# Optimization experiments

Measured on AMD Instinct MI355X. Metric: run time of the kernel, lower is better.

The kernel has to match this reference:

```python
import jax, jax.numpy as jnp
import numpy as np


def setup_inputs() -> dict:
    key = jax.random.key(0)
    k1, k2 = jax.random.split(key)
    qs = jax.random.normal(k1, (64, 32, 128), dtype=jnp.float32)   # (n_queries, n_query_tokens, dim)
    ps = jax.random.normal(k2, (64, 1024, 128), dtype=jnp.float32)  # (n_docs, n_doc_tokens, dim)
    return {"qs": qs, "ps": ps}


def reference(qs, ps):
    # ColBERT MaxSim: for each (query b, doc c), sum over query tokens of the
    # max similarity against all doc tokens.
    # scores[b,c,n,s] = sum_d qs[b,n,d] * ps[c,s,d]
    sim = jnp.einsum('bnd,csd->bcns', qs, ps)  # (n_q, n_d, tok_q, tok_d)
    scores = sim.max(axis=3).sum(axis=2)       # (n_q, n_d)
    return scores
```

## Files before the change

kernel.cpp:

```cpp
#include <hip/hip_runtime.h>
#include <stdint.h>


typedef __bf16 bf16x8 __attribute__((ext_vector_type(8)));
typedef float floatx16 __attribute__((ext_vector_type(16)));

#define QS_N (64u * 32u * 128u)
#define PS_N (64u * 1024u * 128u)

__device__ ushort g_bf[QS_N + PS_N];

__global__ __launch_bounds__(256) void cvt_kernel(const float* __restrict__ qs,
                                                  const float* __restrict__ ps) {
  const int nq4 = QS_N / 4;
  const int n4 = (QS_N + PS_N) / 4;
  int i = blockIdx.x * 256 + threadIdx.x;
  if (i >= n4) return;
  float4 f = (i < nq4) ? ((const float4*)qs)[i] : ((const float4*)ps)[i - nq4];
  union { ushort4 s; struct { __bf16 a, b, c, d; } h; } o;
  o.h.a = (__bf16)f.x; o.h.b = (__bf16)f.y; o.h.c = (__bf16)f.z; o.h.d = (__bf16)f.w;
  ((ushort4*)g_bf)[i] = o.s;
}

__device__ inline float rmax16(const floatx16& a) {
  float m0 = fmaxf(fmaxf(a[0], a[1]), fmaxf(a[2], a[3]));
  float m1 = fmaxf(fmaxf(a[4], a[5]), fmaxf(a[6], a[7]));
  float m2 = fmaxf(fmaxf(a[8], a[9]), fmaxf(a[10], a[11]));
  float m3 = fmaxf(fmaxf(a[12], a[13]), fmaxf(a[14], a[15]));
  return fmaxf(fmaxf(m0, m1), fmaxf(m2, m3));
}

typedef __attribute__((address_space(1))) const void gas_t;
typedef __attribute__((address_space(3))) void las_t;
__device__ inline void gload_lds16(const ushort* g, ushort* l) {
  __builtin_amdgcn_global_load_lds((gas_t*)g, (las_t*)l, 16, 0, 0);
}

#define ZERO16 {0, 0, 0, 0, 0, 0, 0, 0, 0, 0, 0, 0, 0, 0, 0, 0}

__global__ __launch_bounds__(256) void maxsim_kernel(float* __restrict__ out) {
  const ushort* qsb = g_bf;
  const ushort* psb = g_bf + QS_N;

  const int lane = threadIdx.x & 63;
  const int wave = threadIdx.x >> 6;

  const int xcd = blockIdx.x & 7;
  const int slot = blockIdx.x >> 3;
  const int c = xcd * 8 + (slot >> 3);
  const int bg = slot & 7;
  const int qb0 = bg * 8 + wave * 2;

  const int row = lane & 31;
  const int hi8 = (lane >> 5) * 8;

  bf16x8 qf[2][8];
#pragma unroll
  for (int bb = 0; bb < 2; ++bb) {
    const ushort* q = qsb + ((qb0 + bb) * 32 + row) * 128 + hi8;
#pragma unroll
    for (int k = 0; k < 8; ++k)
      qf[bb][k] = *(const bf16x8*)(q + k * 16);
  }

  __shared__ __align__(16) ushort lds_p[2][4096];

  const int pg_lane = (c * 1024 + row) * 128 + hi8;

#pragma unroll
  for (int jj = 0; jj < 2; ++jj) {
    const int j = wave * 2 + jj;
    gload_lds16(psb + pg_lane + j * 16, &lds_p[0][j * 512]);
  }
  __syncthreads();

  float vmax0 = -3.4e38f, vmax1 = -3.4e38f;
  int cb = 0;

#pragma unroll 1
  for (int t = 0; t < 32; ++t) {
    if (t < 31) {
      const int soff = (t + 1) * 32 * 128;
#pragma unroll
      for (int jj = 0; jj < 2; ++jj) {
        const int j = wave * 2 + jj;
        gload_lds16(psb + pg_lane + soff + j * 16, &lds_p[cb ^ 1][j * 512]);
      }
    }
    const ushort* lp = &lds_p[cb][0] + lane * 8;
    floatx16 acc0 = ZERO16, acc1 = ZERO16;
#pragma unroll
    for (int k = 0; k < 8; ++k) {
      bf16x8 af = *(const bf16x8*)(lp + k * 512);
      acc0 = __builtin_amdgcn_mfma_f32_32x32x16_bf16(af, qf[0][k], acc0, 0, 0, 0);
      acc1 = __builtin_amdgcn_mfma_f32_32x32x16_bf16(af, qf[1][k], acc1, 0, 0, 0);
    }
    vmax0 = fmaxf(vmax0, rmax16(acc0));
    vmax1 = fmaxf(vmax1, rmax16(acc1));
    __syncthreads();
    cb ^= 1;
  }

  vmax0 = fmaxf(vmax0, __shfl_xor(vmax0, 32, 64));
  vmax1 = fmaxf(vmax1, __shfl_xor(vmax1, 32, 64));
#pragma unroll
  for (int o = 16; o > 0; o >>= 1) {
    vmax0 += __shfl_xor(vmax0, o, 64);
    vmax1 += __shfl_xor(vmax1, o, 64);
  }
  if (lane == 0) {
    out[(qb0 + 0) * 64 + c] = vmax0;
    out[(qb0 + 1) * 64 + c] = vmax1;
  }
}

extern "C" void kernel_launch(void* const* d_in, const int* in_sizes, int n_in,
                              void* d_out, int out_size, void* d_ws, size_t ws_size,
                              hipStream_t stream) {
  const float* qs = (const float*)d_in[0];
  const float* ps = (const float*)d_in[1];
  float* out = (float*)d_out;
  (void)d_ws; (void)ws_size;

  const int n4 = (int)((QS_N + PS_N) / 4);
  cvt_kernel<<<(n4 + 255) / 256, 256, 0, stream>>>(qs, ps);
  maxsim_kernel<<<dim3(512), dim3(256), 0, stream>>>(out);
}
```

Baseline: 111.5 us.

## Fuse fp32-to-bf16 conversion into the MaxSim kernel and drop the separate pass

Removes the standalone conversion kernel and its bf16 scratch buffer. The MaxSim kernel now loads fp32 queries and documents directly and converts them to bf16 in registers. Document tiles are prefetched into registers during the MFMA loop and written to LDS after compute, replacing async global-to-LDS loads. This trades an extra launch and a full round trip of the converted data for doubled redundant fp32 traffic across blocks that share a document, and for register-staged prefetching.

```diff
diff --git a/kernel.cpp b/kernel.cpp
--- a/kernel.cpp
+++ b/kernel.cpp
@@ -5,21 +5,11 @@
 typedef __bf16 bf16x8 __attribute__((ext_vector_type(8)));
 typedef float floatx16 __attribute__((ext_vector_type(16)));
 
-#define QS_N (64u * 32u * 128u)
-#define PS_N (64u * 1024u * 128u)
-
-__device__ ushort g_bf[QS_N + PS_N];
-
-__global__ __launch_bounds__(256) void cvt_kernel(const float* __restrict__ qs,
-                                                  const float* __restrict__ ps) {
-  const int nq4 = QS_N / 4;
-  const int n4 = (QS_N + PS_N) / 4;
-  int i = blockIdx.x * 256 + threadIdx.x;
-  if (i >= n4) return;
-  float4 f = (i < nq4) ? ((const float4*)qs)[i] : ((const float4*)ps)[i - nq4];
-  union { ushort4 s; struct { __bf16 a, b, c, d; } h; } o;
-  o.h.a = (__bf16)f.x; o.h.b = (__bf16)f.y; o.h.c = (__bf16)f.z; o.h.d = (__bf16)f.w;
-  ((ushort4*)g_bf)[i] = o.s;
+__device__ inline bf16x8 cvt8(const float4& a, const float4& b) {
+  bf16x8 r;
+  r[0] = (__bf16)a.x; r[1] = (__bf16)a.y; r[2] = (__bf16)a.z; r[3] = (__bf16)a.w;
+  r[4] = (__bf16)b.x; r[5] = (__bf16)b.y; r[6] = (__bf16)b.z; r[7] = (__bf16)b.w;
+  return r;
 }
 
 __device__ inline float rmax16(const floatx16& a) {
@@ -30,18 +20,11 @@
   return fmaxf(fmaxf(m0, m1), fmaxf(m2, m3));
 }
 
-typedef __attribute__((address_space(1))) const void gas_t;
-typedef __attribute__((address_space(3))) void las_t;
-__device__ inline void gload_lds16(const ushort* g, ushort* l) {
-  __builtin_amdgcn_global_load_lds((gas_t*)g, (las_t*)l, 16, 0, 0);
-}
-
 #define ZERO16 {0, 0, 0, 0, 0, 0, 0, 0, 0, 0, 0, 0, 0, 0, 0, 0}
 
-__global__ __launch_bounds__(256) void maxsim_kernel(float* __restrict__ out) {
-  const ushort* qsb = g_bf;
-  const ushort* psb = g_bf + QS_N;
-
+__global__ __launch_bounds__(256) void maxsim_kernel(const float* __restrict__ qs,
+                                                     const float* __restrict__ ps,
+                                                     float* __restrict__ out) {
   const int lane = threadIdx.x & 63;
   const int wave = threadIdx.x >> 6;
 
@@ -57,20 +40,26 @@
   bf16x8 qf[2][8];
 #pragma unroll
   for (int bb = 0; bb < 2; ++bb) {
-    const ushort* q = qsb + ((qb0 + bb) * 32 + row) * 128 + hi8;
+    const float* q = qs + ((qb0 + bb) * 32 + row) * 128 + hi8;
 #pragma unroll
-    for (int k = 0; k < 8; ++k)
-      qf[bb][k] = *(const bf16x8*)(q + k * 16);
+    for (int k = 0; k < 8; ++k) {
+      float4 a = *(const float4*)(q + k * 16);
+      float4 b = *(const float4*)(q + k * 16 + 4);
+      qf[bb][k] = cvt8(a, b);
+    }
   }
 
   __shared__ __align__(16) ushort lds_p[2][4096];
 
-  const int pg_lane = (c * 1024 + row) * 128 + hi8;
+  const float* pg = ps + (c * 1024 + row) * 128 + hi8;
 
 #pragma unroll
   for (int jj = 0; jj < 2; ++jj) {
     const int j = wave * 2 + jj;
-    gload_lds16(psb + pg_lane + j * 16, &lds_p[0][j * 512]);
+    const float* src = pg + j * 16;
+    float4 a = *(const float4*)src;
+    float4 b = *(const float4*)(src + 4);
+    *(bf16x8*)(&lds_p[0][j * 512 + lane * 8]) = cvt8(a, b);
   }
   __syncthreads();
 
@@ -79,13 +68,13 @@
 
 #pragma unroll 1
   for (int t = 0; t < 32; ++t) {
+    float4 Fa0, Fb0, Fa1, Fb1;
     if (t < 31) {
-      const int soff = (t + 1) * 32 * 128;
-#pragma unroll
-      for (int jj = 0; jj < 2; ++jj) {
-        const int j = wave * 2 + jj;
-        gload_lds16(psb + pg_lane + soff + j * 16, &lds_p[cb ^ 1][j * 512]);
-      }
+      const float* src = pg + (t + 1) * 32 * 128 + (wave * 2) * 16;
+      Fa0 = *(const float4*)src;
+      Fb0 = *(const float4*)(src + 4);
+      Fa1 = *(const float4*)(src + 16);
+      Fb1 = *(const float4*)(src + 20);
     }
     const ushort* lp = &lds_p[cb][0] + lane * 8;
     floatx16 acc0 = ZERO16, acc1 = ZERO16;
@@ -97,6 +86,11 @@
     }
     vmax0 = fmaxf(vmax0, rmax16(acc0));
     vmax1 = fmaxf(vmax1, rmax16(acc1));
+    if (t < 31) {
+      ushort* dst = &lds_p[cb ^ 1][(wave * 2) * 512 + lane * 8];
+      *(bf16x8*)dst = cvt8(Fa0, Fb0);
+      *(bf16x8*)(dst + 512) = cvt8(Fa1, Fb1);
+    }
     __syncthreads();
     cb ^= 1;
   }
@@ -122,7 +116,5 @@
   float* out = (float*)d_out;
   (void)d_ws; (void)ws_size;
 
-  const int n4 = (int)((QS_N + PS_N) / 4);
-  cvt_kernel<<<(n4 + 255) / 256, 256, 0, stream>>>(qs, ps);
-  maxsim_kernel<<<dim3(512), dim3(256), 0, stream>>>(out);
+  maxsim_kernel<<<dim3(512), dim3(256), 0, stream>>>(qs, ps, out);
 }
```

After: 124.5 us. 11.7% more time.

## Split doc tokens across wave pairs, each wave holds four query blocks

Applied to the files above, without the earlier changes.

Each wave now keeps four query blocks in registers instead of two. Pairs of waves take different 32-token halves of a 64-token doc tile, so each LDS A-fragment load feeds four MFMAs and the loop runs 16 iterations instead of 32. A shared-memory cross-wave max reduction merges the two halves before the final sum. Per-wave register pressure doubles, which is pinned with empty asm constraints, and the LDS buffer doubles in size, which may reduce occupancy.

```diff
diff --git a/kernel.cpp b/kernel.cpp
--- a/kernel.cpp
+++ b/kernel.cpp
@@ -9,6 +9,8 @@
 #define PS_N (64u * 1024u * 128u)
 
 __device__ ushort g_bf[QS_N + PS_N];
+
+union FU { bf16x8 v; uint4 u; };
 
 __global__ __launch_bounds__(256) void cvt_kernel(const float* __restrict__ qs,
                                                   const float* __restrict__ ps) {
@@ -49,68 +51,93 @@
   const int slot = blockIdx.x >> 3;
   const int c = xcd * 8 + (slot >> 3);
   const int bg = slot & 7;
-  const int qb0 = bg * 8 + wave * 2;
+
+  const int qgrp = wave >> 1;
+  const int usel = wave & 1;
+  const int qb0 = bg * 8 + qgrp * 4;
 
   const int row = lane & 31;
   const int hi8 = (lane >> 5) * 8;
 
-  bf16x8 qf[2][8];
+  uint4 qf[4][8];
 #pragma unroll
-  for (int bb = 0; bb < 2; ++bb) {
+  for (int bb = 0; bb < 4; ++bb) {
     const ushort* q = qsb + ((qb0 + bb) * 32 + row) * 128 + hi8;
 #pragma unroll
     for (int k = 0; k < 8; ++k)
-      qf[bb][k] = *(const bf16x8*)(q + k * 16);
+      qf[bb][k] = *(const uint4*)(q + k * 16);
   }
+#pragma unroll
+  for (int bb = 0; bb < 4; ++bb)
+#pragma unroll
+    for (int k = 0; k < 8; ++k)
+      asm volatile("" : "+v"(qf[bb][k].x), "+v"(qf[bb][k].y),
+                        "+v"(qf[bb][k].z), "+v"(qf[bb][k].w));
 
-  __shared__ __align__(16) ushort lds_p[2][4096];
+  __shared__ __align__(16) ushort lds_p[2][8192];
 
   const int pg_lane = (c * 1024 + row) * 128 + hi8;
 
-#pragma unroll
-  for (int jj = 0; jj < 2; ++jj) {
-    const int j = wave * 2 + jj;
-    gload_lds16(psb + pg_lane + j * 16, &lds_p[0][j * 512]);
+#define STAGE(L, tt)                                                          \
+  _Pragma("unroll") for (int jj = 0; jj < 4; ++jj) {                          \
+    const int m = wave * 4 + jj;                                              \
+    const int u = m >> 3, j = m & 7;                                          \
+    gload_lds16(psb + pg_lane + (tt) * 8192 + u * 32 * 128 + j * 16,          \
+                (L) + u * 4096 + j * 512);                                    \
   }
+
+  STAGE(&lds_p[0][0], 0)
   __syncthreads();
 
-  float vmax0 = -3.4e38f, vmax1 = -3.4e38f;
+  float vmax[4];
+#pragma unroll
+  for (int bb = 0; bb < 4; ++bb) vmax[bb] = -3.4e38f;
   int cb = 0;
 
 #pragma unroll 1
-  for (int t = 0; t < 32; ++t) {
-    if (t < 31) {
-      const int soff = (t + 1) * 32 * 128;
-#pragma unroll
-      for (int jj = 0; jj < 2; ++jj) {
-        const int j = wave * 2 + jj;
-        gload_lds16(psb + pg_lane + soff + j * 16, &lds_p[cb ^ 1][j * 512]);
-      }
+  for (int t = 0; t < 16; ++t) {
+    if (t < 15) {
+      STAGE(&lds_p[cb ^ 1][0], t + 1)
     }
-    const ushort* lp = &lds_p[cb][0] + lane * 8;
-    floatx16 acc0 = ZERO16, acc1 = ZERO16;
+    const ushort* lp = &lds_p[cb][usel * 4096] + lane * 8;
+    floatx16 a0 = ZERO16, a1 = ZERO16, a2 = ZERO16, a3 = ZERO16;
 #pragma unroll
     for (int k = 0; k < 8; ++k) {
       bf16x8 af = *(const bf16x8*)(lp + k * 512);
-      acc0 = __builtin_amdgcn_mfma_f32_32x32x16_bf16(af, qf[0][k], acc0, 0, 0, 0);
-      acc1 = __builtin_amdgcn_mfma_f32_32x32x16_bf16(af, qf[1][k], acc1, 0, 0, 0);
+      FU f0; f0.u = qf[0][k];
+      FU f1; f1.u = qf[1][k];
+      FU f2; f2.u = qf[2][k];
+      FU f3; f3.u = qf[3][k];
+      a0 = __builtin_amdgcn_mfma_f32_32x32x16_bf16(af, f0.v, a0, 0, 0, 0);
+      a1 = __builtin_amdgcn_mfma_f32_32x32x16_bf16(af, f1.v, a1, 0, 0, 0);
+      a2 = __builtin_amdgcn_mfma_f32_32x32x16_bf16(af, f2.v, a2, 0, 0, 0);
+      a3 = __builtin_amdgcn_mfma_f32_32x32x16_bf16(af, f3.v, a3, 0, 0, 0);
     }
-    vmax0 = fmaxf(vmax0, rmax16(acc0));
-    vmax1 = fmaxf(vmax1, rmax16(acc1));
+    vmax[0] = fmaxf(vmax[0], rmax16(a0));
+    vmax[1] = fmaxf(vmax[1], rmax16(a1));
+    vmax[2] = fmaxf(vmax[2], rmax16(a2));
+    vmax[3] = fmaxf(vmax[3], rmax16(a3));
     __syncthreads();
     cb ^= 1;
   }
 
-  vmax0 = fmaxf(vmax0, __shfl_xor(vmax0, 32, 64));
-  vmax1 = fmaxf(vmax1, __shfl_xor(vmax1, 32, 64));
 #pragma unroll
-  for (int o = 16; o > 0; o >>= 1) {
-    vmax0 += __shfl_xor(vmax0, o, 64);
-    vmax1 += __shfl_xor(vmax1, o, 64);
+  for (int bb = 0; bb < 4; ++bb)
+    vmax[bb] = fmaxf(vmax[bb], __shfl_xor(vmax[bb], 32, 64));
+
+  __shared__ float red[4][4][32];
+  if (lane < 32) {
+#pragma unroll
+    for (int bb = 0; bb < 4; ++bb) red[wave][bb][lane] = vmax[bb];
   }
-  if (lane == 0) {
-    out[(qb0 + 0) * 64 + c] = vmax0;
-    out[(qb0 + 1) * 64 + c] = vmax1;
+  __syncthreads();
+  {
+    const int q = threadIdx.x >> 5;
+    const int n = threadIdx.x & 31;
+    float m = fmaxf(red[(q >> 2) * 2][q & 3][n], red[(q >> 2) * 2 + 1][q & 3][n]);
+#pragma unroll
+    for (int o = 16; o > 0; o >>= 1) m += __shfl_xor(m, o, 32);
+    if (n == 0) out[(bg * 8 + q) * 64 + c] = m;
   }
 }
 
```

Result: slower. 115.1 us (+3.2%).
